# Performance work log

Measured on AMD Instinct MI355X. Metric: run time of the kernel, lower is better.

## Reference

```python
import jax, jax.numpy as jnp
import numpy as np

HIDDEN = 128


def setup_inputs() -> dict:
    key = jax.random.key(0)
    ks = jax.random.split(key, 16)
    n_agents, n_regions = 1024, 1024
    agent_dim, region_dim, h = 24, 20, HIDDEN

    def rn(k, shape, scale=0.05):
        return jax.random.normal(k, shape, dtype=jnp.float32) * scale

    return {
        "x_agent": jax.random.normal(ks[0], (n_agents, agent_dim), dtype=jnp.float32),
        "x_region": jax.random.normal(ks[1], (n_regions, region_dim), dtype=jnp.float32),
        "Wa1": rn(ks[2], (agent_dim, h)), "ba1": rn(ks[3], (h,)),
        "Wa2": rn(ks[4], (h, h)), "ba2": rn(ks[5], (h,)),
        "Wr1": rn(ks[6], (region_dim, h)), "br1": rn(ks[7], (h,)),
        "Wr2": rn(ks[8], (h, h)), "br2": rn(ks[9], (h,)),
        "Ws1": rn(ks[10], (2 * h, h)), "bs1": rn(ks[11], (h,)),
        "Ws2": rn(ks[12], (h, 1)), "bs2": rn(ks[13], (1,)),
    }


def reference(x_agent, x_region, Wa1, ba1, Wa2, ba2, Wr1, br1, Wr2, br2,
              Ws1, bs1, Ws2, bs2):
    # Agent / region encoder MLPs: Linear -> ReLU -> Linear -> ReLU
    agent_emb = jax.nn.relu(jax.nn.relu(x_agent @ Wa1 + ba1) @ Wa2 + ba2)    # [A, H]
    region_emb = jax.nn.relu(jax.nn.relu(x_region @ Wr1 + br1) @ Wr2 + br2)  # [R, H]

    # score_head on concat([a_exp, r_exp]) == split Ws1 into agent/region halves
    # and broadcast-sum the two projections; avoids materializing [A, R, 2H].
    h = agent_emb.shape[-1]
    Ws1_a, Ws1_r = Ws1[:h], Ws1[h:]                # each [H, H]
    pa = agent_emb @ Ws1_a                          # [A, H]
    pr = region_emb @ Ws1_r                         # [R, H]
    pair_h = jax.nn.relu(pa[:, None, :] + pr[None, :, :] + bs1)  # [A, R, H]
    scores = jnp.einsum("arh,ho->aro", pair_h, Ws2)[..., 0] + bs2[0]  # [A, R]
    return scores
```

## Files before the change

kernel.cpp:

```cpp
#include <hip/hip_runtime.h>

#define H 128

typedef float f2 __attribute__((ext_vector_type(2)));

__global__ __launch_bounds__(128) void emb_kernel(
    const float* __restrict__ xA, const float* __restrict__ xR,
    const float* __restrict__ Wa1, const float* __restrict__ ba1,
    const float* __restrict__ Wa2, const float* __restrict__ ba2,
    const float* __restrict__ Wr1, const float* __restrict__ br1,
    const float* __restrict__ Wr2, const float* __restrict__ br2,
    const float* __restrict__ Ws1, const float* __restrict__ bs1,
    float* __restrict__ pa, float* __restrict__ pr,
    int na, int nr)
{
    const int ROWS = 8;
    const int b = blockIdx.x;
    const int nblkA = na / ROWS;
    const bool isA = (b < nblkA);
    const int row0 = (isA ? b : b - nblkA) * ROWS;
    const float* __restrict__ x  = isA ? xA : xR;
    const float* __restrict__ W1 = isA ? Wa1 : Wr1;
    const float* __restrict__ b1 = isA ? ba1 : br1;
    const float* __restrict__ W2 = isA ? Wa2 : Wr2;
    const float* __restrict__ b2 = isA ? ba2 : br2;
    const float* __restrict__ W3 = isA ? Ws1 : Ws1 + H * H;
    float* __restrict__ outp     = isA ? pa : pr;
    const int in_dim = isA ? 24 : 20;

    __shared__ float sX[ROWS][24];
    __shared__ float sH[ROWS][H];

    const int j = threadIdx.x;

    #pragma unroll
    for (int t = 0; t < 2; ++t) {
        int idx = t * 128 + j;
        if (idx < ROWS * 24) {
            int r = idx / 24, k = idx - r * 24;
            sX[r][k] = (k < in_dim) ? x[(row0 + r) * in_dim + k] : 0.f;
        }
    }
    __syncthreads();

    float w1[24];
    #pragma unroll
    for (int k = 0; k < 24; ++k)
        w1[k] = (k < in_dim) ? W1[k * H + j] : 0.f;
    {
        const float bj = b1[j];
        #pragma unroll
        for (int r = 0; r < ROWS; ++r) {
            float s = bj;
            #pragma unroll
            for (int k = 0; k < 24; ++k) s += sX[r][k] * w1[k];
            sH[r][j] = fmaxf(s, 0.f);
        }
    }
    __syncthreads();

    float acc[ROWS];
    {
        const float bj = b2[j];
        #pragma unroll
        for (int r = 0; r < ROWS; ++r) acc[r] = bj;
    }
    #pragma unroll
    for (int kc = 0; kc < H; kc += 32) {
        float w2[32];
        #pragma unroll
        for (int kk = 0; kk < 32; ++kk) w2[kk] = W2[(kc + kk) * H + j];
        #pragma unroll
        for (int r = 0; r < ROWS; ++r) {
            float s = acc[r];
            #pragma unroll
            for (int kk = 0; kk < 32; ++kk) s += sH[r][kc + kk] * w2[kk];
            acc[r] = s;
        }
    }
    __syncthreads();
    #pragma unroll
    for (int r = 0; r < ROWS; ++r) sH[r][j] = fmaxf(acc[r], 0.f);
    __syncthreads();

    {
        const float init = isA ? bs1[j] : 0.f;
        #pragma unroll
        for (int r = 0; r < ROWS; ++r) acc[r] = init;
    }
    #pragma unroll
    for (int kc = 0; kc < H; kc += 32) {
        float w3[32];
        #pragma unroll
        for (int kk = 0; kk < 32; ++kk) w3[kk] = W3[(kc + kk) * H + j];
        #pragma unroll
        for (int r = 0; r < ROWS; ++r) {
            float s = acc[r];
            #pragma unroll
            for (int kk = 0; kk < 32; ++kk) s += sH[r][kc + kk] * w3[kk];
            acc[r] = s;
        }
    }
    #pragma unroll
    for (int r = 0; r < ROWS; ++r) outp[(row0 + r) * H + j] = acc[r];
}

__global__ __launch_bounds__(256) void pair_kernel(
    const float* __restrict__ pa, const float* __restrict__ pr,
    const float* __restrict__ Ws2, const float* __restrict__ bs2,
    float* __restrict__ out, int nr)
{
    __shared__ float sA[64 * H];
    __shared__ float sB[64 * H];

    const int tid = threadIdx.x;
    const int a0 = blockIdx.y * 64;
    const int r0 = blockIdx.x * 64;

    const float4* pa4 = (const float4*)pa;
    const float4* pr4 = (const float4*)pr;
    #pragma unroll
    for (int i = 0; i < 8; ++i) {
        int idx = i * 256 + tid;
        int row = idx >> 5;
        int c4  = idx & 31;
        int p   = (c4 ^ (row & 7)) << 2;
        *(float4*)&sA[row * H + p] = pa4[(a0 + row) * (H / 4) + c4];
        *(float4*)&sB[row * H + p] = pr4[(r0 + row) * (H / 4) + c4];
    }
    __syncthreads();

    const int tx = tid & 15;
    const int ty = tid >> 4;

    int rowA[4], rowB[4];
    #pragma unroll
    for (int i = 0; i < 4; ++i) rowA[i] = ty * 4 + i;
    #pragma unroll
    for (int j = 0; j < 4; ++j) rowB[j] = tx + 16 * j;

    f2 acc[4][4];
    #pragma unroll
    for (int i = 0; i < 4; ++i)
        #pragma unroll
        for (int j = 0; j < 4; ++j) acc[i][j] = (f2){0.f, 0.f};

    const float4* w4 = (const float4*)Ws2;
    const f2 zero = {0.f, 0.f};

    #pragma unroll 4
    for (int h4 = 0; h4 < H / 4; ++h4) {
        float4 wv = w4[h4];
        f2 wlo = {wv.x, wv.y}, whi = {wv.z, wv.w};
        float4 av[4], bv[4];
        #pragma unroll
        for (int i = 0; i < 4; ++i)
            av[i] = *(const float4*)&sA[rowA[i] * H + ((h4 ^ (rowA[i] & 7)) << 2)];
        #pragma unroll
        for (int j = 0; j < 4; ++j)
            bv[j] = *(const float4*)&sB[rowB[j] * H + ((h4 ^ (rowB[j] & 7)) << 2)];
        #pragma unroll
        for (int i = 0; i < 4; ++i) {
            f2 alo = {av[i].x, av[i].y}, ahi = {av[i].z, av[i].w};
            #pragma unroll
            for (int j = 0; j < 4; ++j) {
                f2 blo = {bv[j].x, bv[j].y}, bhi = {bv[j].z, bv[j].w};
                f2 zlo = __builtin_elementwise_max(alo + blo, zero);
                f2 zhi = __builtin_elementwise_max(ahi + bhi, zero);
                acc[i][j] += zlo * wlo;
                acc[i][j] += zhi * whi;
            }
        }
    }

    const float b2v = bs2[0];
    #pragma unroll
    for (int i = 0; i < 4; ++i) {
        int a = a0 + rowA[i];
        #pragma unroll
        for (int j = 0; j < 4; ++j) {
            out[(long)a * nr + (r0 + rowB[j])] = acc[i][j].x + acc[i][j].y + b2v;
        }
    }
}

extern "C" void kernel_launch(void* const* d_in, const int* in_sizes, int n_in,
                              void* d_out, int out_size, void* d_ws, size_t ws_size,
                              hipStream_t stream) {
    const float* xA  = (const float*)d_in[0];
    const float* xR  = (const float*)d_in[1];
    const float* Wa1 = (const float*)d_in[2];
    const float* ba1 = (const float*)d_in[3];
    const float* Wa2 = (const float*)d_in[4];
    const float* ba2 = (const float*)d_in[5];
    const float* Wr1 = (const float*)d_in[6];
    const float* br1 = (const float*)d_in[7];
    const float* Wr2 = (const float*)d_in[8];
    const float* br2 = (const float*)d_in[9];
    const float* Ws1 = (const float*)d_in[10];
    const float* bs1 = (const float*)d_in[11];
    const float* Ws2 = (const float*)d_in[12];
    const float* bs2 = (const float*)d_in[13];
    float* out = (float*)d_out;

    const int na = in_sizes[0] / 24;
    const int nr = in_sizes[1] / 20;

    float* pa = (float*)d_ws;
    float* pr = pa + (size_t)na * H;

    emb_kernel<<<dim3(na / 8 + nr / 8), 128, 0, stream>>>(
        xA, xR, Wa1, ba1, Wa2, ba2, Wr1, br1, Wr2, br2, Ws1, bs1, pa, pr, na, nr);

    pair_kernel<<<dim3(nr / 64, na / 64), 256, 0, stream>>>(
        pa, pr, Ws2, bs2, out, nr);
}
```

Before: 106.6 us.

## Read agent projections from global memory in pair kernel and vectorize MLP LDS reads

The pair kernel no longer stages the 64x128 agent tile in shared memory. Each thread loads its four agent rows directly from global memory as float4, relying on the cache, since the 16 threads with the same ty read identical addresses. This halves LDS usage per block, which may allow more resident blocks, but it puts global loads inside the inner loop. The embedding kernel also reads shared memory as float4 instead of scalar loads.

```diff
diff --git a/kernel.cpp b/kernel.cpp
--- a/kernel.cpp
+++ b/kernel.cpp
@@ -28,8 +28,8 @@
     float* __restrict__ outp     = isA ? pa : pr;
     const int in_dim = isA ? 24 : 20;
 
-    __shared__ float sX[ROWS][24];
-    __shared__ float sH[ROWS][H];
+    __shared__ __align__(16) float sX[ROWS][24];
+    __shared__ __align__(16) float sH[ROWS][H];
 
     const int j = threadIdx.x;
 
@@ -51,9 +51,16 @@
         const float bj = b1[j];
         #pragma unroll
         for (int r = 0; r < ROWS; ++r) {
+            const float4* sx4 = (const float4*)&sX[r][0];
             float s = bj;
             #pragma unroll
-            for (int k = 0; k < 24; ++k) s += sX[r][k] * w1[k];
+            for (int k4 = 0; k4 < 6; ++k4) {
+                float4 xv = sx4[k4];
+                s += xv.x * w1[k4 * 4 + 0];
+                s += xv.y * w1[k4 * 4 + 1];
+                s += xv.z * w1[k4 * 4 + 2];
+                s += xv.w * w1[k4 * 4 + 3];
+            }
             sH[r][j] = fmaxf(s, 0.f);
         }
     }
@@ -72,9 +79,16 @@
         for (int kk = 0; kk < 32; ++kk) w2[kk] = W2[(kc + kk) * H + j];
         #pragma unroll
         for (int r = 0; r < ROWS; ++r) {
+            const float4* sh4 = (const float4*)&sH[r][kc];
             float s = acc[r];
             #pragma unroll
-            for (int kk = 0; kk < 32; ++kk) s += sH[r][kc + kk] * w2[kk];
+            for (int k4 = 0; k4 < 8; ++k4) {
+                float4 hv = sh4[k4];
+                s += hv.x * w2[k4 * 4 + 0];
+                s += hv.y * w2[k4 * 4 + 1];
+                s += hv.z * w2[k4 * 4 + 2];
+                s += hv.w * w2[k4 * 4 + 3];
+            }
             acc[r] = s;
         }
     }
@@ -95,9 +109,16 @@
         for (int kk = 0; kk < 32; ++kk) w3[kk] = W3[(kc + kk) * H + j];
         #pragma unroll
         for (int r = 0; r < ROWS; ++r) {
+            const float4* sh4 = (const float4*)&sH[r][kc];
             float s = acc[r];
             #pragma unroll
-            for (int kk = 0; kk < 32; ++kk) s += sH[r][kc + kk] * w3[kk];
+            for (int k4 = 0; k4 < 8; ++k4) {
+                float4 hv = sh4[k4];
+                s += hv.x * w3[k4 * 4 + 0];
+                s += hv.y * w3[k4 * 4 + 1];
+                s += hv.z * w3[k4 * 4 + 2];
+                s += hv.w * w3[k4 * 4 + 3];
+            }
             acc[r] = s;
         }
     }
@@ -110,14 +131,12 @@
     const float* __restrict__ Ws2, const float* __restrict__ bs2,
     float* __restrict__ out, int nr)
 {
-    __shared__ float sA[64 * H];
     __shared__ float sB[64 * H];
 
     const int tid = threadIdx.x;
     const int a0 = blockIdx.y * 64;
     const int r0 = blockIdx.x * 64;
 
-    const float4* pa4 = (const float4*)pa;
     const float4* pr4 = (const float4*)pr;
     #pragma unroll
     for (int i = 0; i < 8; ++i) {
@@ -125,19 +144,21 @@
         int row = idx >> 5;
         int c4  = idx & 31;
         int p   = (c4 ^ (row & 7)) << 2;
-        *(float4*)&sA[row * H + p] = pa4[(a0 + row) * (H / 4) + c4];
         *(float4*)&sB[row * H + p] = pr4[(r0 + row) * (H / 4) + c4];
     }
     __syncthreads();
 
     const int tx = tid & 15;
     const int ty = tid >> 4;
-
-    int rowA[4], rowB[4];
-    #pragma unroll
-    for (int i = 0; i < 4; ++i) rowA[i] = ty * 4 + i;
-    #pragma unroll
-    for (int j = 0; j < 4; ++j) rowB[j] = tx + 16 * j;
+    const int sw7 = tx & 7;
+
+    const float4* pa4 = (const float4*)pa;
+    long aBase[4];
+    #pragma unroll
+    for (int i = 0; i < 4; ++i) aBase[i] = (long)(a0 + ty * 4 + i) * (H / 4);
+    int bBase[4];
+    #pragma unroll
+    for (int j = 0; j < 4; ++j) bBase[j] = (tx + 16 * j) * H;
 
     f2 acc[4][4];
     #pragma unroll
@@ -152,13 +173,14 @@
     for (int h4 = 0; h4 < H / 4; ++h4) {
         float4 wv = w4[h4];
         f2 wlo = {wv.x, wv.y}, whi = {wv.z, wv.w};
+        const int sw = (h4 ^ sw7) << 2;
         float4 av[4], bv[4];
         #pragma unroll
         for (int i = 0; i < 4; ++i)
-            av[i] = *(const float4*)&sA[rowA[i] * H + ((h4 ^ (rowA[i] & 7)) << 2)];
+            av[i] = pa4[aBase[i] + h4];
         #pragma unroll
         for (int j = 0; j < 4; ++j)
-            bv[j] = *(const float4*)&sB[rowB[j] * H + ((h4 ^ (rowB[j] & 7)) << 2)];
+            bv[j] = *(const float4*)&sB[bBase[j] + sw];
         #pragma unroll
         for (int i = 0; i < 4; ++i) {
             f2 alo = {av[i].x, av[i].y}, ahi = {av[i].z, av[i].w};
@@ -176,10 +198,10 @@
     const float b2v = bs2[0];
     #pragma unroll
     for (int i = 0; i < 4; ++i) {
-        int a = a0 + rowA[i];
+        int a = a0 + ty * 4 + i;
         #pragma unroll
         for (int j = 0; j < 4; ++j) {
-            out[(long)a * nr + (r0 + rowB[j])] = acc[i][j].x + acc[i][j].y + b2v;
+            out[(long)a * nr + (r0 + tx + 16 * j)] = acc[i][j].x + acc[i][j].y + b2v;
         }
     }
 }
```

Measured after the change: 104.7 us. Within noise of the previous version (-1.8%).
